# Kernel optimization log

Measured on AMD Instinct MI355X. Metric: run time of the kernel, lower is better.

The kernel has to match this reference:

```python
import jax, jax.numpy as jnp
import numpy as np

N, T, C, H, W = 4, 8, 512, 14, 14
HEADS = 8
D = C // HEADS            # 64 per-head dim
S = T * H * W             # 1568 sequence length
EPS = 1e-8
NEG = -2.0**32 + 1.0      # padding value used by the original module


def setup_inputs() -> dict:
    key = jax.random.key(0)
    ks = jax.random.split(key, 8)
    shp = (N, T, C, H, W)
    scale = 1.0 / np.sqrt(C)
    return {
        "queries": jax.random.normal(ks[0], shp, jnp.float32),
        "keys": jax.random.normal(ks[1], shp, jnp.float32),
        "values": jax.random.normal(ks[2], shp, jnp.float32),
        "Wq": jax.random.normal(ks[3], (C, C), jnp.float32) * scale,
        "bq": jnp.zeros((C,), jnp.float32),
        "Wk": jax.random.normal(ks[4], (C, C), jnp.float32) * scale,
        "bk": jnp.zeros((C,), jnp.float32),
        "Wv": jax.random.normal(ks[5], (C, C), jnp.float32) * scale,
        "bv": jnp.zeros((C,), jnp.float32),
        "gamma": jnp.ones((C,), jnp.float32),
        "beta": jnp.zeros((C,), jnp.float32),
    }


def _proj(x, Wt, b):
    # 1x1 Conv2d + ReLU over channel dim of (N, T, C, H, W)
    y = jnp.einsum('ntchw,oc->ntohw', x, Wt) + b[None, None, :, None, None]
    return jax.nn.relu(y)


def _flatten(x):
    # (N, T, C, H, W) -> (N, T*H*W, C)
    return x.transpose(0, 1, 3, 4, 2).reshape(N, S, C)


def _split_heads(x):
    # torch.cat(torch.chunk(x, HEADS, dim=2), dim=0): (N, S, C) -> (HEADS*N, S, D)
    return x.reshape(N, S, HEADS, D).transpose(2, 0, 1, 3).reshape(HEADS * N, S, D)


def reference(queries, keys, values, Wq, bq, Wk, bk, Wv, bv, gamma, beta):
    Qf = _flatten(_proj(queries, Wq, bq))
    Kf = _flatten(_proj(keys, Wk, bk))
    Vf = _flatten(_proj(values, Wv, bv))
    q_flat = _flatten(queries)   # residual + query mask source
    k_flat = _flatten(keys)      # key mask source

    Q_ = _split_heads(Qf)
    K_ = _split_heads(Kf)
    V_ = _split_heads(Vf)

    scores = jnp.einsum('bqd,bkd->bqk', Q_, K_) / jnp.sqrt(jnp.float32(D))

    # key padding mask: sign(|sum over C|), tiled over heads -> (HEADS*N, 1, S)
    key_mask = jnp.sign(jnp.abs(k_flat.sum(-1)))          # (N, S)
    km = jnp.tile(key_mask, (HEADS, 1))[:, None, :]
    scores = jnp.where(km == 0.0, NEG, scores)

    attn = jax.nn.softmax(scores, axis=-1)

    # query padding mask (multiplicative) -> (HEADS*N, S, 1)
    query_mask = jnp.sign(jnp.abs(q_flat.sum(-1)))        # (N, S)
    qm = jnp.tile(query_mask, (HEADS, 1))[:, :, None]
    attn = attn * qm

    out = jnp.einsum('bqk,bkd->bqd', attn, V_)
    # merge heads back: inverse of _split_heads
    out = out.reshape(HEADS, N, S, D).transpose(1, 2, 0, 3).reshape(N, S, C)

    out = out + q_flat  # residual

    # custom LayerNorm: torch .std() is unbiased (ddof=1)
    mean = out.mean(-1, keepdims=True)
    std = jnp.sqrt(out.var(-1, ddof=1, keepdims=True))
    out = gamma * (out - mean) / (std + EPS) + beta

    # reshape back to (N, T, C, H, W)
    return out.reshape(N, T, H, W, C).transpose(0, 1, 4, 2, 3)
```

## Files before the change

kernel.cpp:

```cpp
#include <hip/hip_runtime.h>
#include <math.h>

#define N_ 4
#define T_ 8
#define C_ 512
#define H_ 14
#define W_ 14
#define HEADS_ 8
#define D_ 64
#define HW_ 196
#define S_ 1568
#define P_TOT 6272
#define KMP_ 1600
#define NEGL_ (-1.0e38f)
#define EPS_ 1e-8f
#define QSC_ 0.18033688011112042f

typedef __attribute__((ext_vector_type(8))) short short8v;
typedef __attribute__((ext_vector_type(4))) float float4v;
typedef __attribute__((ext_vector_type(4))) unsigned short ushort4v;
typedef unsigned short ushort_t;

__device__ __forceinline__ ushort_t f2bf(float f) {
    union { float f; unsigned u; } a; a.f = f;
    unsigned r = (a.u + 0x7FFFu + ((a.u >> 16) & 1u)) >> 16;
    return (ushort_t)r;
}
__device__ __forceinline__ float bf2f(ushort_t u) {
    union { unsigned u; float f; } t; t.u = ((unsigned)u) << 16; return t.f;
}
__device__ __forceinline__ unsigned cvt_pk_bf16(float lo, float hi) {
    unsigned r;
    asm("v_cvt_pk_bf16_f32 %0, %1, %2" : "=v"(r) : "v"(lo), "v"(hi));
    return r;
}
__device__ __forceinline__ float exp2_fast(float x) {
    float r;
    asm("v_exp_f32 %0, %1" : "=v"(r) : "v"(x));
    return r;
}
__device__ __forceinline__ float4v mfma16(short8v a, short8v b, float4v c) {
    return __builtin_amdgcn_mfma_f32_16x16x32_bf16(a, b, c, 0, 0, 0);
}
__device__ __forceinline__ void gload_lds16(const void* g, void* l) {
    __builtin_amdgcn_global_load_lds(
        (const __attribute__((address_space(1))) unsigned int*)g,
        (__attribute__((address_space(3))) unsigned int*)l,
        16, 0, 0);
}
__device__ __forceinline__ void gload_lds4(const void* g, void* l) {
    __builtin_amdgcn_global_load_lds(
        (const __attribute__((address_space(1))) unsigned int*)g,
        (__attribute__((address_space(3))) unsigned int*)l,
        4, 0, 0);
}

__global__ __launch_bounds__(256) void transpose_kernel(
    const float* __restrict__ q_in, const float* __restrict__ k_in,
    const float* __restrict__ v_in, ushort_t* __restrict__ qbf,
    ushort_t* __restrict__ kbf, ushort_t* __restrict__ vbf,
    const float* __restrict__ Wq, const float* __restrict__ Wk,
    const float* __restrict__ Wv, ushort_t* __restrict__ Wbf)
{
    __shared__ float Xs[64][197];
    const int z = blockIdx.z;
    const int nt = blockIdx.x;
    const int ct = blockIdx.y;
    const int tid = threadIdx.x;

    if (z == 3) {
        const int blk = nt * 8 + ct;
        #pragma unroll
        for (int i = 0; i < 3; ++i) {
            const int q = (blk * 3 + i) * 256 + tid;
            const int zi = q >> 16;
            const int qi = q & 65535;
            const float* src = (zi == 0) ? Wq : (zi == 1) ? Wk : Wv;
            const float4 v = *(const float4*)(src + qi * 4);
            ushort4v pk;
            pk[0] = f2bf(v.x); pk[1] = f2bf(v.y);
            pk[2] = f2bf(v.z); pk[3] = f2bf(v.w);
            *(ushort4v*)(Wbf + (long)zi * 262144 + qi * 4) = pk;
        }
        return;
    }

    const float* src = (z == 0) ? q_in : (z == 1) ? k_in : v_in;
    ushort_t* dst = (z == 0) ? qbf : (z == 1) ? kbf : vbf;

    const long gbase = ((long)nt * C_ + ct * 64) * HW_;
    #pragma unroll
    for (int i = 0; i < 13; ++i) {
        const int idx = i * 256 + tid;
        if (idx < 3136) {
            const int c = idx / 49;
            const int q4 = idx - c * 49;
            const float4 v = *(const float4*)(src + gbase + c * HW_ + q4 * 4);
            Xs[c][q4 * 4 + 0] = v.x;
            Xs[c][q4 * 4 + 1] = v.y;
            Xs[c][q4 * 4 + 2] = v.z;
            Xs[c][q4 * 4 + 3] = v.w;
        }
    }
    __syncthreads();
    const long pbase = (long)nt * HW_;
    const int c0 = (tid & 15) * 4;
    #pragma unroll
    for (int i = 0; i < 13; ++i) {
        const int idx = i * 256 + tid;
        if (idx < 3136) {
            const int hw = idx >> 4;
            ushort4v pk;
            #pragma unroll
            for (int e = 0; e < 4; ++e) pk[e] = f2bf(Xs[c0 + e][hw]);
            *(ushort4v*)(dst + (pbase + hw) * C_ + ct * 64 + c0) = pk;
        }
    }
}

__global__ __launch_bounds__(256) void mask_kernel(
    const ushort_t* __restrict__ qbf, const ushort_t* __restrict__ kbf,
    float* __restrict__ qm, float* __restrict__ km)
{
    const int tid = threadIdx.x;
    const int w = tid >> 6, lane = tid & 63;
    const int p = blockIdx.x * 4 + w;
    const short8v qv = *(const short8v*)(qbf + (long)p * C_ + lane * 8);
    const short8v kv = *(const short8v*)(kbf + (long)p * C_ + lane * 8);
    float sq = 0.f, sk = 0.f;
    #pragma unroll
    for (int j = 0; j < 8; ++j) {
        sq += bf2f(((const ushort_t*)&qv)[j]);
        sk += bf2f(((const ushort_t*)&kv)[j]);
    }
    #pragma unroll
    for (int off = 32; off > 0; off >>= 1) {
        sq += __shfl_xor(sq, off, 64);
        sk += __shfl_xor(sk, off, 64);
    }
    if (lane == 0) {
        const int n = p / S_, s = p - n * S_;
        qm[p] = (sq != 0.f) ? 1.f : 0.f;
        km[n * KMP_ + s] = (sk != 0.f) ? 0.f : NEGL_;
    }
    if (blockIdx.x == 0 && tid < 128) {
        const int nn = tid >> 5;
        const int ss = S_ + (tid & 31);
        km[nn * KMP_ + ss] = NEGL_;
    }
}

__global__ __launch_bounds__(256) void proj_all(
    const ushort_t* __restrict__ qbf, const ushort_t* __restrict__ kbf,
    const ushort_t* __restrict__ vbf, const ushort_t* __restrict__ Wbf,
    const float* __restrict__ bq, const float* __restrict__ bk,
    const float* __restrict__ bv,
    ushort_t* __restrict__ Qh, ushort_t* __restrict__ Kh,
    ushort_t* __restrict__ Vt)
{
    __shared__ char lds[49152];

    const int fid = blockIdx.x;
    const int xcd = fid & 7;
    const int iin = fid >> 3;
    const int v = xcd * 147 + iin;
    const int z = v / 392;
    const int rem = v - z * 392;
    const int ptile = rem >> 3;
    const int head = rem & 7;

    const ushort_t* Xbf = (z == 0) ? qbf : (z == 1) ? kbf : vbf;
    const ushort_t* Wz = Wbf + (long)z * 262144;
    const float* bias = (z == 0) ? bq : (z == 1) ? bk : bv;
    ushort_t* outp = (z == 0) ? Qh : (z == 1) ? Kh : Vt;
    const bool TR = (z == 2);
    const float osc = (z == 0) ? QSC_ : 1.0f;

    const int tid = threadIdx.x;
    const int w = tid >> 6, lane = tid & 63, lg = lane >> 4, lo = lane & 15;
    const int wr = w >> 1, wc = w & 1;
    const int p0 = ptile * 128;
    const int o0 = head * 64;

    const int wbase = (tid & 192) * 16;

    float4v acc[2][4];
    #pragma unroll
    for (int a = 0; a < 2; ++a)
        #pragma unroll
        for (int b = 0; b < 4; ++b) acc[a][b] = (float4v){0.f, 0.f, 0.f, 0.f};

    auto stage = [&](int buf, int k0) {
        char* Xl = lds + buf * 24576;
        char* Wl = Xl + 16384;
        #pragma unroll
        for (int i = 0; i < 4; ++i) {
            const int sl = tid + i * 256;
            const int row = sl >> 3, sir = sl & 7;
            const int c16 = sir ^ (row & 7);
            gload_lds16(Xbf + (long)(p0 + row) * C_ + k0 + c16 * 8,
                        Xl + i * 4096 + wbase);
        }
        #pragma unroll
        for (int i = 0; i < 2; ++i) {
            const int sl = tid + i * 256;
            const int row = sl >> 3, sir = sl & 7;
            const int c16 = sir ^ (row & 7);
            gload_lds16(Wz + (long)(o0 + row) * C_ + k0 + c16 * 8,
                        Wl + i * 4096 + wbase);
        }
    };

    stage(0, 0);
    #pragma unroll
    for (int kstep = 0; kstep < 8; ++kstep) {
        __syncthreads();
        if (kstep < 7) stage((kstep + 1) & 1, (kstep + 1) * 64);

        const char* Xl = lds + (kstep & 1) * 24576;
        const char* Wl = Xl + 16384;
        short8v wf[2][2], xf[4][2];
        #pragma unroll
        for (int a = 0; a < 2; ++a) {
            const int row = wc * 32 + a * 16 + lo;
            const int swr = (row & 7) << 4;
            #pragma unroll
            for (int ks = 0; ks < 2; ++ks) {
                const int base = row * 128 + ks * 64 + lg * 8;
                ((uint2*)&wf[a][ks])[0] = *(const uint2*)(Wl + (base ^ swr));
                ((uint2*)&wf[a][ks])[1] = *(const uint2*)(Wl + ((base + 32) ^ swr));
            }
        }
        #pragma unroll
        for (int b = 0; b < 4; ++b) {
            const int row = wr * 64 + b * 16 + lo;
            const int swr = (row & 7) << 4;
            #pragma unroll
            for (int ks = 0; ks < 2; ++ks) {
                const int base = row * 128 + ks * 64 + lg * 8;
                ((uint2*)&xf[b][ks])[0] = *(const uint2*)(Xl + (base ^ swr));
                ((uint2*)&xf[b][ks])[1] = *(const uint2*)(Xl + ((base + 32) ^ swr));
            }
        }
        __builtin_amdgcn_s_setprio(1);
        if (!TR) {
            #pragma unroll
            for (int ks = 0; ks < 2; ++ks)
                #pragma unroll
                for (int a = 0; a < 2; ++a)
                    #pragma unroll
                    for (int b = 0; b < 4; ++b)
                        acc[a][b] = mfma16(wf[a][ks], xf[b][ks], acc[a][b]);
        } else {
            #pragma unroll
            for (int ks = 0; ks < 2; ++ks)
                #pragma unroll
                for (int a = 0; a < 2; ++a)
                    #pragma unroll
                    for (int b = 0; b < 4; ++b)
                        acc[a][b] = mfma16(xf[b][ks], wf[a][ks], acc[a][b]);
        }
        __builtin_amdgcn_s_setprio(0);
    }

    if (!TR) {
        #pragma unroll
        for (int b = 0; b < 4; ++b) {
            const int p = p0 + wr * 64 + b * 16 + lo;
            const int nb = p / S_;
            const int s = p - nb * S_;
            #pragma unroll
            for (int a = 0; a < 2; ++a) {
                const int d0 = wc * 32 + a * 16 + lg * 4;
                const float4v bs = *(const float4v*)(bias + o0 + d0);
                ushort4v pk;
                #pragma unroll
                for (int e = 0; e < 4; ++e) {
                    float vv = acc[a][b][e] + bs[e];
                    vv = vv > 0.f ? vv : 0.f;
                    pk[e] = f2bf(vv * osc);
                }
                *(ushort4v*)(outp + ((long)(head * N_ + nb) * S_ + s) * D_ + d0) = pk;
            }
        }
    } else {
        #pragma unroll
        for (int a = 0; a < 2; ++a) {
            const int d = wc * 32 + a * 16 + lo;
            const float bsc = bias[o0 + d];
            #pragma unroll
            for (int b = 0; b < 4; ++b) {
                const int pb = p0 + wr * 64 + b * 16 + lg * 4;
                const int nb = pb / S_;
                const int s0 = pb - nb * S_;
                ushort4v pk;
                #pragma unroll
                for (int e = 0; e < 4; ++e) {
                    float vv = acc[a][b][e] + bsc;
                    vv = vv > 0.f ? vv : 0.f;
                    pk[e] = f2bf(vv);
                }
                *(ushort4v*)(outp + ((long)(head * N_ + nb) * D_ + d) * S_ + s0) = pk;
            }
        }
    }
}

__global__ __launch_bounds__(256) void attn_kernel(
    const ushort_t* __restrict__ Qh, const ushort_t* __restrict__ Kh,
    const ushort_t* __restrict__ Vt, const float* __restrict__ km,
    ushort_t* __restrict__ Pc, float* __restrict__ Lp)
{
    __shared__ char lds[16384 + 256];

    const int tid = threadIdx.x;
    const int lane = tid & 63;
    const int w = tid >> 6;
    const int lg = lane >> 4;
    const int lo = lane & 15;

    const int split = blockIdx.y;
    const int t1 = 7 + split * 6;
    const int t0 = split ? (1 + split * 6) : 0;

    const int fid = blockIdx.x;
    const int x = fid & 7;
    const int j = fid >> 3;
    const int b = x + 8 * (j / 25);
    const int q0 = (j % 25) * 64;
    const int n = b & (N_ - 1);

    char* Kl = lds;
    char* Vl = lds + 8192;
    const float* kms = (const float*)(lds + 16384);
    const int wbase = (tid & 192) * 16;

    const int qrow = q0 + w * 16 + lo;
    const int qcl = qrow < S_ ? qrow : S_ - 1;
    const ushort_t* qp = Qh + ((long)b * S_ + qcl) * D_ + lg * 4;
    short8v qf[2];
    #pragma unroll
    for (int ks = 0; ks < 2; ++ks) {
        ((uint2*)&qf[ks])[0] = *(const uint2*)(qp + ks * 32);
        ((uint2*)&qf[ks])[1] = *(const uint2*)(qp + ks * 32 + 16);
    }

    float4v acc[4];
    #pragma unroll
    for (int dt = 0; dt < 4; ++dt) acc[dt] = (float4v){0.f, 0.f, 0.f, 0.f};
    float l_run = 0.f;

    auto stageK = [&](int kb) {
        #pragma unroll
        for (int i = 0; i < 2; ++i) {
            const int s = i * 256 + tid;
            const int row = s >> 3;
            const int c16 = (s & 7) ^ (row & 7);
            int krow = kb + row; if (krow >= S_) krow = S_ - 1;
            gload_lds16(Kh + ((long)b * S_ + krow) * D_ + c16 * 8,
                        Kl + i * 4096 + wbase);
        }
        if (w == 0)
            gload_lds4(km + (long)n * KMP_ + kb + lane, (void*)kms);
    };
    auto stageV = [&](int kb) {
        #pragma unroll
        for (int i = 0; i < 2; ++i) {
            const int s = i * 256 + tid;
            const int row = s >> 3;
            const int c16 = (s & 7) ^ (row & 7);
            int kc = kb + c16 * 8; if (kc > S_ - 8) kc = S_ - 8;
            gload_lds16(Vt + ((long)b * D_ + row) * S_ + kc,
                        Vl + i * 4096 + wbase);
        }
    };

    for (int t = t0; t < t1; ++t) {
        stageK(t * 64);
        stageV(t * 64);
        asm volatile("s_waitcnt vmcnt(2)" ::: "memory");
        __builtin_amdgcn_s_barrier();

        float4v s[4];
        __builtin_amdgcn_s_setprio(1);
        #pragma unroll
        for (int kt = 0; kt < 4; ++kt) {
            s[kt] = (float4v){0.f, 0.f, 0.f, 0.f};
            #pragma unroll
            for (int ks = 0; ks < 2; ++ks) {
                const int row = kt * 16 + lo;
                const int base = row * 128 + ks * 64 + lg * 8;
                const int swr = (row & 7) << 4;
                short8v kf;
                ((uint2*)&kf)[0] = *(const uint2*)(Kl + (base ^ swr));
                ((uint2*)&kf)[1] = *(const uint2*)(Kl + ((base + 32) ^ swr));
                s[kt] = mfma16(kf, qf[ks], s[kt]);
            }
        }
        __builtin_amdgcn_s_setprio(0);

        float p[4][4];
        #pragma unroll
        for (int kt = 0; kt < 4; ++kt) {
            const float4v bv4 = *(const float4v*)&kms[kt * 16 + lg * 4];
            #pragma unroll
            for (int r = 0; r < 4; ++r)
                p[kt][r] = exp2_fast(s[kt][r] + bv4[r]);
        }
        float rs4[4];
        #pragma unroll
        for (int kt = 0; kt < 4; ++kt)
            rs4[kt] = (p[kt][0] + p[kt][1]) + (p[kt][2] + p[kt][3]);
        l_run += (rs4[0] + rs4[1]) + (rs4[2] + rs4[3]);

        short8v pf[2];
        #pragma unroll
        for (int kt = 0; kt < 4; ++kt) {
            const unsigned w0 = cvt_pk_bf16(p[kt][0], p[kt][1]);
            const unsigned w1 = cvt_pk_bf16(p[kt][2], p[kt][3]);
            ((unsigned*)&pf[kt >> 1])[(kt & 1) * 2] = w0;
            ((unsigned*)&pf[kt >> 1])[(kt & 1) * 2 + 1] = w1;
        }

        asm volatile("s_waitcnt vmcnt(0)" ::: "memory");
        __builtin_amdgcn_s_barrier();

        __builtin_amdgcn_s_setprio(1);
        #pragma unroll
        for (int dt = 0; dt < 4; ++dt) {
            #pragma unroll
            for (int ks = 0; ks < 2; ++ks) {
                const int row = dt * 16 + lo;
                const int base = row * 128 + ks * 64 + lg * 8;
                const int swr = (row & 7) << 4;
                short8v vf;
                ((uint2*)&vf)[0] = *(const uint2*)(Vl + (base ^ swr));
                ((uint2*)&vf)[1] = *(const uint2*)(Vl + ((base + 32) ^ swr));
                acc[dt] = mfma16(vf, pf[ks], acc[dt]);
            }
        }
        __builtin_amdgcn_s_setprio(0);
        __syncthreads();
    }

    l_run += __shfl_xor(l_run, 16, 64);
    l_run += __shfl_xor(l_run, 32, 64);

    if (qrow < S_) {
        const long rbase = ((long)split * 32 + b) * S_ + qrow;
        if (lg == 0) Lp[rbase] = l_run;
        ushort_t* P = Pc + rbase * 64;
        #pragma unroll
        for (int dt = 0; dt < 4; ++dt) {
            uint2 uu;
            uu.x = cvt_pk_bf16(acc[dt][0], acc[dt][1]);
            uu.y = cvt_pk_bf16(acc[dt][2], acc[dt][3]);
            *(uint2*)(P + dt * 16 + lg * 4) = uu;
        }
    }
}

__global__ __launch_bounds__(256) void combine_ln_kernel(
    const ushort_t* __restrict__ Pc, const float* __restrict__ Lp,
    const float* __restrict__ qm, const ushort_t* __restrict__ qbf,
    const float* __restrict__ gamma, const float* __restrict__ beta,
    ushort_t* __restrict__ Om)
{
    const int tid = threadIdx.x;
    const int wv = tid >> 6, lane = tid & 63;
    const long pos = (long)blockIdx.x * 4 + wv;
    const int n = (int)(pos / S_);
    const int q = (int)(pos - (long)n * S_);
    const int head = lane >> 3;
    const int d0 = (lane & 7) * 8;

    float L = 0.f;
    float o[8] = {0.f, 0.f, 0.f, 0.f, 0.f, 0.f, 0.f, 0.f};
    #pragma unroll
    for (int s = 0; s < 4; ++s) {
        const long rb = ((long)(s * 32 + head * 4 + n) * S_ + q);
        L += Lp[rb];
        const ushort4v a0 = *(const ushort4v*)(Pc + rb * 64 + d0);
        const ushort4v a1 = *(const ushort4v*)(Pc + rb * 64 + d0 + 4);
        #pragma unroll
        for (int e = 0; e < 4; ++e) {
            o[e] += bf2f(a0[e]);
            o[4 + e] += bf2f(a1[e]);
        }
    }
    L = fmaxf(L, 1e-20f);
    const float scale = qm[pos] / L;
    const short8v qv = *(const short8v*)(qbf + pos * C_ + lane * 8);
    float v8[8];
    float sum = 0.f, ssq = 0.f;
    #pragma unroll
    for (int e = 0; e < 8; ++e) {
        const float v = o[e] * scale + bf2f(((const ushort_t*)&qv)[e]);
        v8[e] = v;
        sum += v; ssq += v * v;
    }
    #pragma unroll
    for (int off = 32; off > 0; off >>= 1) {
        sum += __shfl_xor(sum, off, 64);
        ssq += __shfl_xor(ssq, off, 64);
    }
    const float mean = sum * (1.f / 512.f);
    float var = (ssq - sum * mean) * (1.f / 511.f);
    var = var > 0.f ? var : 0.f;
    const float inv = 1.f / (sqrtf(var) + EPS_);

    const float4v g0 = *(const float4v*)(gamma + lane * 8);
    const float4v g1 = *(const float4v*)(gamma + lane * 8 + 4);
    const float4v b0 = *(const float4v*)(beta + lane * 8);
    const float4v b1 = *(const float4v*)(beta + lane * 8 + 4);
    ushort4v ov0, ov1;
    #pragma unroll
    for (int e = 0; e < 4; ++e) {
        ov0[e] = f2bf(g0[e] * (v8[e] - mean) * inv + b0[e]);
        ov1[e] = f2bf(g1[e] * (v8[4 + e] - mean) * inv + b1[e]);
    }
    *(ushort4v*)(Om + pos * C_ + lane * 8) = ov0;
    *(ushort4v*)(Om + pos * C_ + lane * 8 + 4) = ov1;
}

__global__ __launch_bounds__(256) void ln_write_kernel(
    const ushort_t* __restrict__ Om, float* __restrict__ out)
{
    __shared__ float Tl[64][197];
    const int nt = blockIdx.x;
    const int ct = blockIdx.y;
    const int tid = threadIdx.x;

    const int c0 = (tid & 15) * 4;
    #pragma unroll
    for (int i = 0; i < 13; ++i) {
        const int idx = i * 256 + tid;
        if (idx < 3136) {
            const int hw = idx >> 4;
            const long p = (long)nt * HW_ + hw;
            const ushort4v ov = *(const ushort4v*)(Om + p * C_ + ct * 64 + c0);
            #pragma unroll
            for (int e = 0; e < 4; ++e) Tl[c0 + e][hw] = bf2f(ov[e]);
        }
    }
    __syncthreads();
    const long obase = ((long)nt * C_ + ct * 64) * HW_;
    #pragma unroll
    for (int i = 0; i < 13; ++i) {
        const int idx = i * 256 + tid;
        if (idx < 3136) {
            const int c = idx / 49;
            const int q4 = idx - c * 49;
            float4 v;
            v.x = Tl[c][q4 * 4 + 0];
            v.y = Tl[c][q4 * 4 + 1];
            v.z = Tl[c][q4 * 4 + 2];
            v.w = Tl[c][q4 * 4 + 3];
            *(float4*)(out + obase + c * HW_ + q4 * 4) = v;
        }
    }
}

extern "C" void kernel_launch(void* const* d_in, const int* in_sizes, int n_in,
                              void* d_out, int out_size, void* d_ws, size_t ws_size,
                              hipStream_t stream) {
    const float* q_in  = (const float*)d_in[0];
    const float* k_in  = (const float*)d_in[1];
    const float* v_in  = (const float*)d_in[2];
    const float* Wq    = (const float*)d_in[3];
    const float* bq    = (const float*)d_in[4];
    const float* Wk    = (const float*)d_in[5];
    const float* bk    = (const float*)d_in[6];
    const float* Wv    = (const float*)d_in[7];
    const float* bv    = (const float*)d_in[8];
    const float* gamma = (const float*)d_in[9];
    const float* beta  = (const float*)d_in[10];
    float* out = (float*)d_out;

    const size_t PC = (size_t)P_TOT * C_;
    ushort_t* qbf = (ushort_t*)d_ws;
    ushort_t* kbf = qbf + PC;
    ushort_t* vbf = kbf + PC;
    ushort_t* Wbf = vbf + PC;
    ushort_t* Qh  = Wbf + 3 * (size_t)C_ * C_;
    ushort_t* Kh  = Qh + PC;
    ushort_t* Vt  = Kh + PC;
    ushort_t* Om  = Vt + PC;
    ushort_t* Pc  = Om + PC;
    float* Lp    = (float*)(Pc + 4L * 32 * S_ * 64);
    float* qm    = Lp + 4L * 32 * S_;
    float* km    = qm + P_TOT;

    transpose_kernel<<<dim3(32, 8, 4), 256, 0, stream>>>(
        q_in, k_in, v_in, qbf, kbf, vbf, Wq, Wk, Wv, Wbf);
    mask_kernel<<<P_TOT / 4, 256, 0, stream>>>(qbf, kbf, qm, km);
    proj_all<<<1176, 256, 0, stream>>>(qbf, kbf, vbf, Wbf, bq, bk, bv, Qh, Kh, Vt);
    attn_kernel<<<dim3(800, 4), 256, 0, stream>>>(Qh, Kh, Vt, km, Pc, Lp);
    combine_ln_kernel<<<P_TOT / 4, 256, 0, stream>>>(Pc, Lp, qm, qbf, gamma, beta, Om);
    ln_write_kernel<<<dim3(32, 8), 256, 0, stream>>>(Om, out);
}
```

Baseline: 94.25 us.

## Halve attention key splits, read key mask from global, fold query mask into LN

Attention now splits the key range in two (13/12 tiles) instead of four, which halves the partial-output buffers and the reads in the combine kernel. The key-mask bias is loaded straight from global memory in the softmax loop instead of being staged into LDS with an extra async load. The query mask is computed inside the combine/LayerNorm kernel from the residual row it already reads, so the mask kernel only handles keys. Fewer splits means 1600 blocks instead of 3200, with longer serial work per block and possibly less latency hiding.

Result: no change. 94.30 us (+0.1%).

```diff
diff --git a/kernel.cpp b/kernel.cpp
--- a/kernel.cpp
+++ b/kernel.cpp
@@ -48,12 +48,6 @@
         (__attribute__((address_space(3))) unsigned int*)l,
         16, 0, 0);
 }
-__device__ __forceinline__ void gload_lds4(const void* g, void* l) {
-    __builtin_amdgcn_global_load_lds(
-        (const __attribute__((address_space(1))) unsigned int*)g,
-        (__attribute__((address_space(3))) unsigned int*)l,
-        4, 0, 0);
-}
 
 __global__ __launch_bounds__(256) void transpose_kernel(
     const float* __restrict__ q_in, const float* __restrict__ k_in,
@@ -119,28 +113,19 @@
 }
 
 __global__ __launch_bounds__(256) void mask_kernel(
-    const ushort_t* __restrict__ qbf, const ushort_t* __restrict__ kbf,
-    float* __restrict__ qm, float* __restrict__ km)
+    const ushort_t* __restrict__ kbf, float* __restrict__ km)
 {
     const int tid = threadIdx.x;
     const int w = tid >> 6, lane = tid & 63;
     const int p = blockIdx.x * 4 + w;
-    const short8v qv = *(const short8v*)(qbf + (long)p * C_ + lane * 8);
     const short8v kv = *(const short8v*)(kbf + (long)p * C_ + lane * 8);
-    float sq = 0.f, sk = 0.f;
-    #pragma unroll
-    for (int j = 0; j < 8; ++j) {
-        sq += bf2f(((const ushort_t*)&qv)[j]);
-        sk += bf2f(((const ushort_t*)&kv)[j]);
-    }
-    #pragma unroll
-    for (int off = 32; off > 0; off >>= 1) {
-        sq += __shfl_xor(sq, off, 64);
-        sk += __shfl_xor(sk, off, 64);
-    }
+    float sk = 0.f;
+    #pragma unroll
+    for (int j = 0; j < 8; ++j) sk += bf2f(((const ushort_t*)&kv)[j]);
+    #pragma unroll
+    for (int off = 32; off > 0; off >>= 1) sk += __shfl_xor(sk, off, 64);
     if (lane == 0) {
         const int n = p / S_, s = p - n * S_;
-        qm[p] = (sq != 0.f) ? 1.f : 0.f;
         km[n * KMP_ + s] = (sk != 0.f) ? 0.f : NEGL_;
     }
     if (blockIdx.x == 0 && tid < 128) {
@@ -311,7 +296,7 @@
     const ushort_t* __restrict__ Vt, const float* __restrict__ km,
     ushort_t* __restrict__ Pc, float* __restrict__ Lp)
 {
-    __shared__ char lds[16384 + 256];
+    __shared__ char lds[16384];
 
     const int tid = threadIdx.x;
     const int lane = tid & 63;
@@ -320,8 +305,8 @@
     const int lo = lane & 15;
 
     const int split = blockIdx.y;
-    const int t1 = 7 + split * 6;
-    const int t0 = split ? (1 + split * 6) : 0;
+    const int t0 = split ? 13 : 0;
+    const int t1 = split ? 25 : 13;
 
     const int fid = blockIdx.x;
     const int x = fid & 7;
@@ -332,8 +317,8 @@
 
     char* Kl = lds;
     char* Vl = lds + 8192;
-    const float* kms = (const float*)(lds + 16384);
     const int wbase = (tid & 192) * 16;
+    const float* kmrow = km + (long)n * KMP_;
 
     const int qrow = q0 + w * 16 + lo;
     const int qcl = qrow < S_ ? qrow : S_ - 1;
@@ -360,8 +345,6 @@
             gload_lds16(Kh + ((long)b * S_ + krow) * D_ + c16 * 8,
                         Kl + i * 4096 + wbase);
         }
-        if (w == 0)
-            gload_lds4(km + (long)n * KMP_ + kb + lane, (void*)kms);
     };
     auto stageV = [&](int kb) {
         #pragma unroll
@@ -402,7 +385,7 @@
         float p[4][4];
         #pragma unroll
         for (int kt = 0; kt < 4; ++kt) {
-            const float4v bv4 = *(const float4v*)&kms[kt * 16 + lg * 4];
+            const float4v bv4 = *(const float4v*)(kmrow + t * 64 + kt * 16 + lg * 4);
             #pragma unroll
             for (int r = 0; r < 4; ++r)
                 p[kt][r] = exp2_fast(s[kt][r] + bv4[r]);
@@ -462,9 +445,8 @@
 
 __global__ __launch_bounds__(256) void combine_ln_kernel(
     const ushort_t* __restrict__ Pc, const float* __restrict__ Lp,
-    const float* __restrict__ qm, const ushort_t* __restrict__ qbf,
-    const float* __restrict__ gamma, const float* __restrict__ beta,
-    ushort_t* __restrict__ Om)
+    const ushort_t* __restrict__ qbf, const float* __restrict__ gamma,
+    const float* __restrict__ beta, ushort_t* __restrict__ Om)
 {
     const int tid = threadIdx.x;
     const int wv = tid >> 6, lane = tid & 63;
@@ -477,7 +459,7 @@
     float L = 0.f;
     float o[8] = {0.f, 0.f, 0.f, 0.f, 0.f, 0.f, 0.f, 0.f};
     #pragma unroll
-    for (int s = 0; s < 4; ++s) {
+    for (int s = 0; s < 2; ++s) {
         const long rb = ((long)(s * 32 + head * 4 + n) * S_ + q);
         L += Lp[rb];
         const ushort4v a0 = *(const ushort4v*)(Pc + rb * 64 + d0);
@@ -489,13 +471,25 @@
         }
     }
     L = fmaxf(L, 1e-20f);
-    const float scale = qm[pos] / L;
+
     const short8v qv = *(const short8v*)(qbf + pos * C_ + lane * 8);
+    float qres[8];
+    float qsum = 0.f;
+    #pragma unroll
+    for (int e = 0; e < 8; ++e) {
+        qres[e] = bf2f(((const ushort_t*)&qv)[e]);
+        qsum += qres[e];
+    }
+    #pragma unroll
+    for (int off = 32; off > 0; off >>= 1) qsum += __shfl_xor(qsum, off, 64);
+    const float qm = (qsum != 0.f) ? 1.f : 0.f;
+    const float scale = qm / L;
+
     float v8[8];
     float sum = 0.f, ssq = 0.f;
     #pragma unroll
     for (int e = 0; e < 8; ++e) {
-        const float v = o[e] * scale + bf2f(((const ushort_t*)&qv)[e]);
+        const float v = o[e] * scale + qres[e];
         v8[e] = v;
         sum += v; ssq += v * v;
     }
@@ -587,15 +581,14 @@
     ushort_t* Vt  = Kh + PC;
     ushort_t* Om  = Vt + PC;
     ushort_t* Pc  = Om + PC;
-    float* Lp    = (float*)(Pc + 4L * 32 * S_ * 64);
-    float* qm    = Lp + 4L * 32 * S_;
-    float* km    = qm + P_TOT;
+    float* Lp    = (float*)(Pc + 2L * 32 * S_ * 64);
+    float* km    = Lp + 2L * 32 * S_;
 
     transpose_kernel<<<dim3(32, 8, 4), 256, 0, stream>>>(
         q_in, k_in, v_in, qbf, kbf, vbf, Wq, Wk, Wv, Wbf);
-    mask_kernel<<<P_TOT / 4, 256, 0, stream>>>(qbf, kbf, qm, km);
+    mask_kernel<<<P_TOT / 4, 256, 0, stream>>>(kbf, km);
     proj_all<<<1176, 256, 0, stream>>>(qbf, kbf, vbf, Wbf, bq, bk, bv, Qh, Kh, Vt);
-    attn_kernel<<<dim3(800, 4), 256, 0, stream>>>(Qh, Kh, Vt, km, Pc, Lp);
-    combine_ln_kernel<<<P_TOT / 4, 256, 0, stream>>>(Pc, Lp, qm, qbf, gamma, beta, Om);
+    attn_kernel<<<dim3(800, 2), 256, 0, stream>>>(Qh, Kh, Vt, km, Pc, Lp);
+    combine_ln_kernel<<<P_TOT / 4, 256, 0, stream>>>(Pc, Lp, qbf, gamma, beta, Om);
     ln_write_kernel<<<dim3(32, 8), 256, 0, stream>>>(Om, out);
 }
```
